# Optimization experiments

Hardware: AMD Instinct MI355X
Metric: run time of the kernel (lower is better)

The kernel has to match this reference:

```python
import jax, jax.numpy as jnp
import numpy as np

OBS, HOR, PD, HID, NH, PROTO = 8, 8, 128, 256, 8, 32
B, N = 8, 4096

def _gelu(x):
    return jax.nn.gelu(x, approximate=False)  # torch nn.GELU default is exact erf

def setup_inputs():
    key = jax.random.key(0)
    ks = iter(jax.random.split(key, 40))
    nrm = lambda shape, s=0.02: jax.random.normal(next(ks), shape, dtype=jnp.float32) * s
    return {
        'obs_points': jax.random.normal(next(ks), (B, N, OBS, 2), dtype=jnp.float32),
        'obs_vis': jax.random.randint(next(ks), (B, N, OBS), 0, 2).astype(bool),
        'rel_xy': jax.random.normal(next(ks), (B, N, 2), dtype=jnp.float32),
        'anchor_obs': jax.random.normal(next(ks), (B, OBS, 2), dtype=jnp.float32),
        'anchor_obs_vel': jax.random.normal(next(ks), (B, OBS, 2), dtype=jnp.float32),
        'semantic_feat': jax.random.normal(next(ks), (B, N, 10), dtype=jnp.float32),
        'ln_w': jnp.ones((OBS * 7,), jnp.float32),
        'ln_b': jnp.zeros((OBS * 7,), jnp.float32),
        'enc_w1': nrm((OBS * 7, PD)), 'enc_b1': jnp.zeros((PD,), jnp.float32),
        'enc_w2': nrm((PD, PD)), 'enc_b2': jnp.zeros((PD,), jnp.float32),
        'time_embed': nrm((HOR, HID)),
        'anchor_w': nrm((OBS * 4, HID)), 'anchor_b': jnp.zeros((HID,), jnp.float32),
        'query_w': nrm((PD, HID)), 'query_b': jnp.zeros((HID,), jnp.float32),
        'in_proj_w': nrm((HID, 3 * HID)), 'in_proj_b': jnp.zeros((3 * HID,), jnp.float32),
        'out_proj_w': nrm((HID, HID)), 'out_proj_b': jnp.zeros((HID,), jnp.float32),
        'ah_w': nrm((HID, 2)), 'ah_b': jnp.zeros((2,), jnp.float32),
        'rh_w1': nrm((HID + PD + 2, HID)), 'rh_b1': jnp.zeros((HID,), jnp.float32),
        'rh_w2': nrm((HID, 2)), 'rh_b2': jnp.zeros((2,), jnp.float32),
        'vh_w1': nrm((HID + PD, HID // 2)), 'vh_b1': jnp.zeros((HID // 2,), jnp.float32),
        'vh_w2': nrm((HID // 2, 1)), 'vh_b2': jnp.zeros((1,), jnp.float32),
        'sh_w': nrm((HID, PROTO)), 'sh_b': jnp.zeros((PROTO,), jnp.float32),
    }

def reference(obs_points, obs_vis, rel_xy, anchor_obs, anchor_obs_vel, semantic_feat,
              ln_w, ln_b, enc_w1, enc_b1, enc_w2, enc_b2, time_embed,
              anchor_w, anchor_b, query_w, query_b, in_proj_w, in_proj_b,
              out_proj_w, out_proj_b, ah_w, ah_b, rh_w1, rh_b1, rh_w2, rh_b2,
              vh_w1, vh_b1, vh_w2, vh_b2, sh_w, sh_b):
    del semantic_feat  # unused, matches original
    Bc, Nc, T, _ = obs_points.shape
    # ---- PointTraceEncoder ----
    vel = jnp.concatenate([jnp.zeros_like(obs_points[:, :, :1]),
                           obs_points[:, :, 1:] - obs_points[:, :, :-1]], axis=2)
    rel = jnp.broadcast_to(rel_xy[:, :, None, :], (Bc, Nc, T, 2))
    feat = jnp.concatenate([obs_points, vel, obs_vis.astype(jnp.float32)[..., None], rel],
                           axis=-1).reshape(Bc, Nc, T * 7)
    mu = feat.mean(-1, keepdims=True)
    var = ((feat - mu) ** 2).mean(-1, keepdims=True)
    x = (feat - mu) / jnp.sqrt(var + 1e-5) * ln_w + ln_b
    point_tokens = _gelu(_gelu(x @ enc_w1 + enc_b1) @ enc_w2 + enc_b2)  # [B,N,PD]
    # ---- queries / memory ----
    anchor_feat = jnp.concatenate([anchor_obs, anchor_obs_vel], -1).reshape(Bc, -1)
    tq = time_embed[None] + (anchor_feat @ anchor_w + anchor_b)[:, None]  # [B,HOR,HID]
    mem = point_tokens @ query_w + query_b  # [B,N,HID]
    # ---- multi-head cross attention ----
    D = tq.shape[-1]; dh = D // NH
    q = tq @ in_proj_w[:, :D] + in_proj_b[:D]
    k = mem @ in_proj_w[:, D:2 * D] + in_proj_b[D:2 * D]
    v = mem @ in_proj_w[:, 2 * D:] + in_proj_b[2 * D:]
    qh = q.reshape(Bc, -1, NH, dh).transpose(0, 2, 1, 3)
    kh = k.reshape(Bc, -1, NH, dh).transpose(0, 2, 1, 3)
    vh = v.reshape(Bc, -1, NH, dh).transpose(0, 2, 1, 3)
    attn = jax.nn.softmax(jnp.einsum('bhqd,bhkd->bhqk', qh, kh) / jnp.sqrt(jnp.float32(dh)), axis=-1)
    o = jnp.einsum('bhqk,bhkd->bhqd', attn, vh).transpose(0, 2, 1, 3).reshape(Bc, -1, D)
    future = o @ out_proj_w + out_proj_b  # [B,HOR,HID]
    # ---- heads ----
    last_anchor = anchor_obs[:, -1]
    anchor_delta = 0.1 * jnp.tanh(future @ ah_w + ah_b)
    anchor_pred = last_anchor[:, None] + jnp.cumsum(anchor_delta, axis=1)  # [B,HOR,2]
    Hq = future.shape[1]
    ft_e = jnp.broadcast_to(future[:, :, None, :], (Bc, Hq, Nc, D))
    pt_e = jnp.broadcast_to(point_tokens[:, None], (Bc, Hq, Nc, point_tokens.shape[-1]))
    rel_e = jnp.broadcast_to(rel_xy[:, None], (Bc, Hq, Nc, 2))
    per_point = jnp.concatenate([ft_e, pt_e, rel_e], axis=-1)  # [B,HOR,N,HID+PD+2]
    residual = 0.1 * jnp.tanh(_gelu(per_point @ rh_w1 + rh_b1) @ rh_w2 + rh_b2)
    pred_points = anchor_pred[:, :, None, :] + residual
    vis_logits = (_gelu(per_point[..., :-2] @ vh_w1 + vh_b1) @ vh_w2 + vh_b2)[..., 0]
    sem_logits = future @ sh_w + sh_b
    return (anchor_pred,
            pred_points.transpose(0, 2, 1, 3),   # [B,N,HOR,2]
            vis_logits.transpose(0, 2, 1),       # [B,N,HOR]
            sem_logits)                           # [B,HOR,PROTO]
```

## Files before the change

### kernel.cpp

```cpp
#include <hip/hip_runtime.h>
#include <math.h>

#define BB 8
#define NN 4096
#define TT 8
#define HORQ 8
#define PD 128
#define HID 256
#define NHD 8
#define DH 32
#define FE 56
#define NC2 16
#define CH2 256

typedef __attribute__((ext_vector_type(8))) short short8;
typedef __attribute__((ext_vector_type(4))) float floatx4;
typedef __attribute__((ext_vector_type(2))) float floatx2;
typedef unsigned short ushort_t;

__device__ __forceinline__ float gelu_fast(float x) {
    float x2 = x * x;
    float y2 = x * fmaf(0.0713551f, x2, 1.5957691f);
    float e = __expf(y2);
    return x - x * __builtin_amdgcn_rcpf(1.f + e);
}

__device__ __forceinline__ float tanh_fast(float x) {
    float e = __expf(2.f * x);
    return 1.f - 2.f * __builtin_amdgcn_rcpf(1.f + e);
}

__device__ __forceinline__ ushort_t f2b(float x) {
    union { float f; unsigned u; } c; c.f = x;
    unsigned r = c.u + 0x7fffu + ((c.u >> 16) & 1u);
    return (ushort_t)(r >> 16);
}
__device__ __forceinline__ float b2f(unsigned hi) {
    union { unsigned u; float f; } c; c.u = hi;
    return c.f;
}

__global__ __launch_bounds__(256) void k_fuse(
    const float* __restrict__ qw, const float* __restrict__ qb,
    const float* __restrict__ ipw, const float* __restrict__ ipb,
    float* __restrict__ Wk, float* __restrict__ Wv,
    float* __restrict__ bk, float* __restrict__ bv)
{
    int j = threadIdx.x;
    int blk = blockIdx.x;
    const float* src = (blk < PD) ? (qw + blk * HID) : qb;
    float sk0 = 0.f, sk1 = 0.f, sk2 = 0.f, sk3 = 0.f;
    float sv0 = 0.f, sv1 = 0.f, sv2 = 0.f, sv3 = 0.f;
    for (int l = 0; l < HID; l += 4) {
        float w0 = src[l], w1 = src[l + 1], w2 = src[l + 2], w3 = src[l + 3];
        sk0 += w0 * ipw[l * 768 + 256 + j];
        sk1 += w1 * ipw[(l + 1) * 768 + 256 + j];
        sk2 += w2 * ipw[(l + 2) * 768 + 256 + j];
        sk3 += w3 * ipw[(l + 3) * 768 + 256 + j];
        sv0 += w0 * ipw[l * 768 + 512 + j];
        sv1 += w1 * ipw[(l + 1) * 768 + 512 + j];
        sv2 += w2 * ipw[(l + 2) * 768 + 512 + j];
        sv3 += w3 * ipw[(l + 3) * 768 + 512 + j];
    }
    float sk = sk0 + sk1 + sk2 + sk3, sv = sv0 + sv1 + sv2 + sv3;
    if (blk < PD) {
        Wk[blk * HID + j] = sk;
        Wv[blk * HID + j] = sv;
    } else {
        bk[j] = sk + ipb[256 + j];
        bv[j] = sv + ipb[512 + j];
    }
}

__global__ __launch_bounds__(256) void k_prep(
    const float* __restrict__ Wk, const float* __restrict__ Wv,
    const float* __restrict__ rw1, const float* __restrict__ vw1,
    const float* __restrict__ w1, const float* __restrict__ w2,
    const float* __restrict__ aobs, const float* __restrict__ avel,
    const float* __restrict__ te, const float* __restrict__ aw, const float* __restrict__ ab,
    const float* __restrict__ ipw, const float* __restrict__ ipb,
    short* __restrict__ Wfrag, short* __restrict__ w1frag, short* __restrict__ w2frag,
    float* __restrict__ qb_)
{
    __shared__ float af[32];
    __shared__ float tqs[HID];
    int tid = threadIdx.x;
    int blk = blockIdx.x;
    int ks = tid >> 6, lane = tid & 63;
    int quad = lane >> 4, c16 = lane & 15;
    if (blk < 56) {
        int nt = blk;
        int n = nt * 16 + c16;
        for (int j = 0; j < 8; j++) {
            int k = ks * 32 + quad * 8 + j;
            float v;
            if (n < 256)      v = Wk[k * HID + n];
            else if (n < 512) v = Wv[k * HID + (n - 256)];
            else if (n < 768) v = rw1[(256 + k) * HID + (n - 512)];
            else              v = vw1[(256 + k) * PD + (n - 768)];
            Wfrag[((nt * 4 + ks) * 64 + lane) * 8 + j] = (short)f2b(v);
        }
    } else if (blk < 64) {
        if (ks < 2) {
            int nt = blk - 56;
            int n = nt * 16 + c16;
            for (int j = 0; j < 8; j++) {
                int k = ks * 32 + quad * 8 + j;
                float v = (k < FE) ? w1[k * PD + n] : 0.f;
                w1frag[((nt * 2 + ks) * 64 + lane) * 8 + j] = (short)f2b(v);
            }
        }
    } else if (blk < 72) {
        int nt = blk - 64;
        int n = nt * 16 + c16;
        for (int j = 0; j < 8; j++) {
            int k = ks * 32 + quad * 8 + j;
            w2frag[((nt * 4 + ks) * 64 + lane) * 8 + j] = (short)f2b(w2[k * PD + n]);
        }
    } else {
        int bh = blk - 72;
        int b = bh >> 3, h = bh & 7;
        if (tid < 32) {
            int t = tid >> 2, m = tid & 3;
            af[tid] = (m < 2) ? aobs[(b * TT + t) * 2 + m] : avel[(b * TT + t) * 2 + (m - 2)];
        }
        __syncthreads();
        float s = te[h * HID + tid] + ab[tid];
        for (int i = 0; i < 32; i++) s += af[i] * aw[i * HID + tid];
        tqs[tid] = s;
        __syncthreads();
        float q0 = ipb[tid], q1 = 0.f, q2 = 0.f, q3 = 0.f;
        for (int i = 0; i < HID; i += 4) {
            q0 += tqs[i] * ipw[i * 768 + tid];
            q1 += tqs[i + 1] * ipw[(i + 1) * 768 + tid];
            q2 += tqs[i + 2] * ipw[(i + 2) * 768 + tid];
            q3 += tqs[i + 3] * ipw[(i + 3) * 768 + tid];
        }
        qb_[(size_t)bh * HID + tid] = q0 + q1 + q2 + q3;
    }
}

#define U1_OFF 0
#define XNB_OFF 17408
#define PTB_OFF 26624
#define RXY_OFF 44032
#define MU_OFF 44544
#define RS_OFF 44800
#define SMEM_BYTES 45056

__global__ __launch_bounds__(256) void k_main(
    const float* __restrict__ obs, const int* __restrict__ vis,
    const float* __restrict__ rel,
    const float* __restrict__ lnw, const float* __restrict__ lnb,
    const float* __restrict__ b1, const float* __restrict__ b2,
    const short* __restrict__ Wfrag, const short* __restrict__ w1frag,
    const short* __restrict__ w2frag,
    const float* __restrict__ bk, const float* __restrict__ bv,
    const float* __restrict__ rw1,
    ushort_t* __restrict__ kb, ushort_t* __restrict__ vb,
    ushort_t* __restrict__ P1, ushort_t* __restrict__ P2)
{
    __shared__ __align__(16) char smem[SMEM_BYTES];
    float* xnf = (float*)(smem + U1_OFF);
    short* h1b = (short*)(smem + U1_OFF);
    short* xnb = (short*)(smem + XNB_OFF);
    short* ptb = (short*)(smem + PTB_OFF);
    float* rxyS = (float*)(smem + RXY_OFF);
    float* muS = (float*)(smem + MU_OFF);
    float* rsS = (float*)(smem + RS_OFF);

    int tid = threadIdx.x;
    int w = tid >> 6, lane = tid & 63;
    int quad = lane >> 4, c16 = lane & 15;
    int bn0 = blockIdx.x * 64;

    #pragma unroll
    for (int u = 0; u < 2; u++) {
        int pair = tid + u * 256;
        int p = pair >> 3, t = pair & 7;
        int bn = bn0 + p;
        float2 oc = *(const float2*)(obs + (bn * TT + t) * 2);
        int tp = t ? (t - 1) : 0;
        float2 op = *(const float2*)(obs + (bn * TT + tp) * 2);
        float dx = t ? (oc.x - op.x) : 0.f;
        float dy = t ? (oc.y - op.y) : 0.f;
        float vv = (float)vis[bn * TT + t];
        float2 rl = *(const float2*)(rel + bn * 2);
        float* xp = xnf + p * 57 + t * 7;
        xp[0] = oc.x; xp[1] = oc.y; xp[2] = dx; xp[3] = dy;
        xp[4] = vv; xp[5] = rl.x; xp[6] = rl.y;
    }
    if (tid < 128) rxyS[tid] = rel[bn0 * 2 + tid];
    __syncthreads();

    {
        int p = tid >> 2, r = tid & 3;
        float s = 0.f, ss = 0.f;
        for (int e = r; e < FE; e += 4) { float v = xnf[p * 57 + e]; s += v; ss += v * v; }
        s += __shfl_xor(s, 1); ss += __shfl_xor(ss, 1);
        s += __shfl_xor(s, 2); ss += __shfl_xor(ss, 2);
        if (r == 0) {
            float mu = s * (1.f / FE);
            float var = ss * (1.f / FE) - mu * mu;
            muS[p] = mu;
            rsS[p] = rsqrtf(var + 1e-5f);
        }
    }
    __syncthreads();

    for (int idx = tid; idx < 64 * 64; idx += 256) {
        int p = idx >> 6, e = idx & 63;
        float v = 0.f;
        if (e < FE) v = (xnf[p * 57 + e] - muS[p]) * rsS[p] * lnw[e] + lnb[e];
        xnb[p * 72 + e] = (short)f2b(v);
    }
    __syncthreads();

    {
        short8 af1[4][2];
        #pragma unroll
        for (int mt = 0; mt < 4; mt++)
            #pragma unroll
            for (int ks = 0; ks < 2; ks++)
                af1[mt][ks] = *(const short8*)(xnb + (mt * 16 + c16) * 72 + ks * 32 + quad * 8);
        #pragma unroll
        for (int ntl = 0; ntl < 2; ntl++) {
            int nt = w * 2 + ntl;
            short8 bf1[2];
            #pragma unroll
            for (int ks = 0; ks < 2; ks++)
                bf1[ks] = *(const short8*)(w1frag + ((nt * 2 + ks) * 64 + lane) * 8);
            int col = nt * 16 + c16;
            float bb = b1[col];
            #pragma unroll
            for (int mt = 0; mt < 4; mt++) {
                floatx4 acc = {0.f, 0.f, 0.f, 0.f};
                acc = __builtin_amdgcn_mfma_f32_16x16x32_bf16(af1[mt][0], bf1[0], acc, 0, 0, 0);
                acc = __builtin_amdgcn_mfma_f32_16x16x32_bf16(af1[mt][1], bf1[1], acc, 0, 0, 0);
                #pragma unroll
                for (int r = 0; r < 4; r++) {
                    int row = mt * 16 + quad * 4 + r;
                    h1b[row * 136 + col] = (short)f2b(gelu_fast(acc[r] + bb));
                }
            }
        }
    }
    __syncthreads();

    {
        short8 af2[4][4];
        #pragma unroll
        for (int mt = 0; mt < 4; mt++)
            #pragma unroll
            for (int ks = 0; ks < 4; ks++)
                af2[mt][ks] = *(const short8*)(h1b + (mt * 16 + c16) * 136 + ks * 32 + quad * 8);
        #pragma unroll
        for (int ntl = 0; ntl < 2; ntl++) {
            int nt = w * 2 + ntl;
            short8 bf2[4];
            #pragma unroll
            for (int ks = 0; ks < 4; ks++)
                bf2[ks] = *(const short8*)(w2frag + ((nt * 4 + ks) * 64 + lane) * 8);
            int col = nt * 16 + c16;
            float bb = b2[col];
            #pragma unroll
            for (int mt = 0; mt < 4; mt++) {
                floatx4 acc = {0.f, 0.f, 0.f, 0.f};
                #pragma unroll
                for (int ks = 0; ks < 4; ks++)
                    acc = __builtin_amdgcn_mfma_f32_16x16x32_bf16(af2[mt][ks], bf2[ks], acc, 0, 0, 0);
                #pragma unroll
                for (int r = 0; r < 4; r++) {
                    int row = mt * 16 + quad * 4 + r;
                    ptb[row * 136 + col] = (short)f2b(gelu_fast(acc[r] + bb));
                }
            }
        }
    }
    __syncthreads();

    {
        short8 af[4][4];
        #pragma unroll
        for (int mt = 0; mt < 4; mt++)
            #pragma unroll
            for (int ks = 0; ks < 4; ks++)
                af[mt][ks] = *(const short8*)(ptb + (mt * 16 + c16) * 136 + ks * 32 + quad * 8);
        for (int i = 0; i < 14; i++) {
            int nt = w + i * 4;
            short8 bf[4];
            #pragma unroll
            for (int ks = 0; ks < 4; ks++)
                bf[ks] = *(const short8*)(Wfrag + ((nt * 4 + ks) * 64 + lane) * 8);
            floatx4 acc[4];
            #pragma unroll
            for (int mt = 0; mt < 4; mt++) {
                acc[mt] = (floatx4){0.f, 0.f, 0.f, 0.f};
                #pragma unroll
                for (int ks = 0; ks < 4; ks++)
                    acc[mt] = __builtin_amdgcn_mfma_f32_16x16x32_bf16(af[mt][ks], bf[ks], acc[mt], 0, 0, 0);
            }
            int n = nt * 16 + c16;
            if (nt < 16) {
                float bb = bk[n];
                #pragma unroll
                for (int mt = 0; mt < 4; mt++)
                    #pragma unroll
                    for (int r = 0; r < 4; r++) {
                        int row = mt * 16 + quad * 4 + r;
                        kb[(size_t)(bn0 + row) * HID + n] = f2b(acc[mt][r] + bb);
                    }
            } else if (nt < 32) {
                int j = n - 256;
                float bb = bv[j];
                #pragma unroll
                for (int mt = 0; mt < 4; mt++)
                    #pragma unroll
                    for (int r = 0; r < 4; r++) {
                        int row = mt * 16 + quad * 4 + r;
                        vb[(size_t)(bn0 + row) * HID + j] = f2b(acc[mt][r] + bb);
                    }
            } else if (nt < 48) {
                int j = n - 512;
                float wr0 = rw1[384 * HID + j], wr1 = rw1[385 * HID + j];
                #pragma unroll
                for (int mt = 0; mt < 4; mt++)
                    #pragma unroll
                    for (int r = 0; r < 4; r++) {
                        int row = mt * 16 + quad * 4 + r;
                        P1[(size_t)(bn0 + row) * HID + j] =
                            f2b(acc[mt][r] + rxyS[row * 2] * wr0 + rxyS[row * 2 + 1] * wr1);
                    }
            } else {
                int j = n - 768;
                #pragma unroll
                for (int mt = 0; mt < 4; mt++)
                    #pragma unroll
                    for (int r = 0; r < 4; r++) {
                        int row = mt * 16 + quad * 4 + r;
                        P2[(size_t)(bn0 + row) * PD + j] = f2b(acc[mt][r]);
                    }
            }
        }
    }
}

__global__ __launch_bounds__(256) void k_att(
    const float* __restrict__ qbuf, const ushort_t* __restrict__ kb, const ushort_t* __restrict__ vbuf,
    float* __restrict__ pm, float* __restrict__ pl, float* __restrict__ po)
{
    __shared__ float sc[8][CH2];
    __shared__ float pos[8][8][DH];
    int tid = threadIdx.x;
    int bidx = blockIdx.x;
    int c = bidx & (NC2 - 1);
    int head = (bidx >> 4) & 7;
    int b = bidx >> 7;
    const float scale = 0.17677669529663688110f;
    {
        int qq = tid >> 5, ln = tid & 31;
        float qr[DH];
        const float* qp = qbuf + (size_t)(b * HORQ + qq) * HID + head * DH;
        #pragma unroll
        for (int u = 0; u < 8; u++) {
            float4 f = *(const float4*)(qp + u * 4);
            qr[u * 4] = f.x; qr[u * 4 + 1] = f.y; qr[u * 4 + 2] = f.z; qr[u * 4 + 3] = f.w;
        }
        #pragma unroll
        for (int i = 0; i < 8; i++) {
            int nn = ln + 32 * i;
            const ushort_t* kp = kb + (size_t)(b * NN + c * CH2 + nn) * HID + head * DH;
            float s = 0.f;
            #pragma unroll
            for (int u = 0; u < 4; u++) {
                uint4 q = *(const uint4*)(kp + u * 8);
                unsigned wd[4] = {q.x, q.y, q.z, q.w};
                #pragma unroll
                for (int t2 = 0; t2 < 4; t2++) {
                    s += qr[u * 8 + 2 * t2]     * b2f(wd[t2] << 16);
                    s += qr[u * 8 + 2 * t2 + 1] * b2f(wd[t2] & 0xffff0000u);
                }
            }
            sc[qq][nn] = s * scale;
        }
    }
    __syncthreads();
    int qq = tid >> 5, r = tid & 31;
    float mx = -1e30f;
    #pragma unroll
    for (int nn = r; nn < CH2; nn += 32) mx = fmaxf(mx, sc[qq][nn]);
    #pragma unroll
    for (int m = 16; m; m >>= 1) mx = fmaxf(mx, __shfl_xor(mx, m, 32));
    float sum = 0.f;
    #pragma unroll
    for (int nn = r; nn < CH2; nn += 32) { float e = __expf(sc[qq][nn] - mx); sc[qq][nn] = e; sum += e; }
    #pragma unroll
    for (int m = 16; m; m >>= 1) sum += __shfl_xor(sum, m, 32);
    if (r == 0) { pm[bidx * 8 + qq] = mx; pl[bidx * 8 + qq] = sum; }
    __syncthreads();
    {
        int g = tid >> 5, d = tid & 31;
        float oacc[8];
        #pragma unroll
        for (int q2 = 0; q2 < 8; q2++) oacc[q2] = 0.f;
        const ushort_t* vp = vbuf + ((size_t)(b * NN + c * CH2 + g * 32)) * HID + head * DH + d;
        for (int i = 0; i < 32; i++) {
            float v = b2f(((unsigned)vp[(size_t)i * HID]) << 16);
            int nn = g * 32 + i;
            #pragma unroll
            for (int q2 = 0; q2 < 8; q2++) oacc[q2] += sc[q2][nn] * v;
        }
        #pragma unroll
        for (int q2 = 0; q2 < 8; q2++) pos[g][q2][d] = oacc[q2];
    }
    __syncthreads();
    {
        int q2 = tid >> 5, d = tid & 31;
        float o = 0.f;
        #pragma unroll
        for (int gg = 0; gg < 8; gg++) o += pos[gg][q2][d];
        po[(size_t)(bidx * 8 + q2) * DH + d] = o;
    }
}

__global__ __launch_bounds__(256) void k_attfut(
    const float* __restrict__ pm, const float* __restrict__ pl, const float* __restrict__ po,
    const float* __restrict__ opw, const float* __restrict__ opb,
    const float* __restrict__ rw1, const float* __restrict__ rb1,
    const float* __restrict__ vw1, const float* __restrict__ vb1,
    const float* __restrict__ shw, const float* __restrict__ shb,
    const float* __restrict__ ahw, const float* __restrict__ ahb,
    float* __restrict__ F1, float* __restrict__ F2, float* __restrict__ dl, float* __restrict__ sem)
{
    __shared__ float orow[HID], fut[HID];
    int tid = threadIdx.x;
    int b = blockIdx.x >> 3, qq = blockIdx.x & 7;
    {
        int head = tid >> 5, d = tid & 31;
        int base = b * 1024 + head * 128 + qq;
        float M = -1e30f;
        #pragma unroll
        for (int c = 0; c < NC2; c++) M = fmaxf(M, pm[base + c * 8]);
        float L = 0.f, o = 0.f;
        #pragma unroll
        for (int c = 0; c < NC2; c++) {
            float wgt = __expf(pm[base + c * 8] - M);
            L += wgt * pl[base + c * 8];
            o += wgt * po[(size_t)(base + c * 8) * DH + d];
        }
        orow[head * DH + d] = o / L;
    }
    __syncthreads();
    {
        float a0 = opb[tid], a1 = 0.f, a2 = 0.f, a3 = 0.f;
        for (int i = 0; i < HID; i += 4) {
            a0 += orow[i] * opw[i * HID + tid];
            a1 += orow[i + 1] * opw[(i + 1) * HID + tid];
            a2 += orow[i + 2] * opw[(i + 2) * HID + tid];
            a3 += orow[i + 3] * opw[(i + 3) * HID + tid];
        }
        fut[tid] = a0 + a1 + a2 + a3;
    }
    __syncthreads();
    int bh = b * HORQ + qq;
    {
        float a0 = rb1[tid], a1 = 0.f, a2 = 0.f, a3 = 0.f;
        for (int i = 0; i < HID; i += 4) {
            a0 += fut[i] * rw1[i * HID + tid];
            a1 += fut[i + 1] * rw1[(i + 1) * HID + tid];
            a2 += fut[i + 2] * rw1[(i + 2) * HID + tid];
            a3 += fut[i + 3] * rw1[(i + 3) * HID + tid];
        }
        F1[(size_t)bh * HID + tid] = a0 + a1 + a2 + a3;
    }
    if (tid < PD) {
        float a0 = vb1[tid], a1 = 0.f, a2 = 0.f, a3 = 0.f;
        for (int i = 0; i < HID; i += 4) {
            a0 += fut[i] * vw1[i * PD + tid];
            a1 += fut[i + 1] * vw1[(i + 1) * PD + tid];
            a2 += fut[i + 2] * vw1[(i + 2) * PD + tid];
            a3 += fut[i + 3] * vw1[(i + 3) * PD + tid];
        }
        F2[(size_t)bh * PD + tid] = a0 + a1 + a2 + a3;
    }
    {
        int j = tid >> 3, part = tid & 7;
        float s3 = 0.f;
        for (int i = part * 32; i < part * 32 + 32; i++) s3 += fut[i] * shw[i * 32 + j];
        s3 += __shfl_xor(s3, 1);
        s3 += __shfl_xor(s3, 2);
        s3 += __shfl_xor(s3, 4);
        if (part == 0) sem[bh * 32 + j] = s3 + shb[j];
    }
    if (tid < 128) {
        int j = tid >> 6, part = tid & 63;
        float a = 0.f;
        #pragma unroll
        for (int u = 0; u < 4; u++) { int i = part * 4 + u; a += fut[i] * ahw[i * 2 + j]; }
        #pragma unroll
        for (int m = 32; m; m >>= 1) a += __shfl_xor(a, m);
        if (part == 0) dl[bh * 2 + j] = 0.1f * tanhf(a + ahb[j]);
    }
}

__global__ void k_cum(const float* __restrict__ aobs, const float* __restrict__ dl, float* __restrict__ out0)
{
    int tid = threadIdx.x;
    if (tid < 16) {
        int b = tid >> 1, c = tid & 1;
        float acc = aobs[(b * TT + 7) * 2 + c];
        for (int h = 0; h < HORQ; h++) {
            acc += dl[(b * HORQ + h) * 2 + c];
            out0[(b * HORQ + h) * 2 + c] = acc;
        }
    }
}

__global__ __launch_bounds__(256) void k_fin(
    const float* __restrict__ F1, const float* __restrict__ F2,
    const ushort_t* __restrict__ P1, const ushort_t* __restrict__ P2,
    const float* __restrict__ rw2, const float* __restrict__ rb2,
    const float* __restrict__ vw2, const float* __restrict__ vb2,
    const float* __restrict__ ap,
    float* __restrict__ out1, float* __restrict__ out2)
{
    int tid = threadIdx.x;
    int sub = tid >> 5;
    int l = tid & 31;
    int bn = blockIdx.x * 8 + sub;
    int b = bn >> 12;

    uint4 q1 = *(const uint4*)(P1 + (size_t)bn * HID + l * 8);
    float p1f[8];
    {
        unsigned wd[4] = {q1.x, q1.y, q1.z, q1.w};
        #pragma unroll
        for (int u = 0; u < 4; u++) {
            p1f[2 * u]     = b2f(wd[u] << 16);
            p1f[2 * u + 1] = b2f(wd[u] & 0xffff0000u);
        }
    }
    floatx2 w01[8];
    {
        const float4* rwp = (const float4*)(rw2 + l * 16);
        #pragma unroll
        for (int u = 0; u < 4; u++) {
            float4 r = rwp[u];
            w01[2 * u] = (floatx2){r.x, r.y};
            w01[2 * u + 1] = (floatx2){r.z, r.w};
        }
    }
    float p2f[4];
    {
        uint2 q2 = *(const uint2*)(P2 + (size_t)bn * PD + l * 4);
        p2f[0] = b2f(q2.x << 16); p2f[1] = b2f(q2.x & 0xffff0000u);
        p2f[2] = b2f(q2.y << 16); p2f[3] = b2f(q2.y & 0xffff0000u);
    }
    float4 wvv = *(const float4*)(vw2 + l * 4);
    float wv[4] = {wvv.x, wvv.y, wvv.z, wvv.w};

    float rb20 = rb2[0], rb21 = rb2[1], vb20 = vb2[0];
    #pragma unroll 2
    for (int h = 0; h < HORQ; h++) {
        const float* f1p = F1 + (size_t)(b * HORQ + h) * HID + l * 8;
        float4 fa = *(const float4*)f1p;
        float4 fb = *(const float4*)(f1p + 4);
        float f1r[8] = {fa.x, fa.y, fa.z, fa.w, fb.x, fb.y, fb.z, fb.w};
        float4 f2v = *(const float4*)(F2 + (size_t)(b * HORQ + h) * PD + l * 4);
        float f2r[4] = {f2v.x, f2v.y, f2v.z, f2v.w};
        floatx2 s01 = {0.f, 0.f};
        float sv = 0.f;
        #pragma unroll
        for (int u = 0; u < 8; u++) {
            float g = gelu_fast(f1r[u] + p1f[u]);
            s01 += (floatx2){g, g} * w01[u];
        }
        #pragma unroll
        for (int u = 0; u < 4; u++) {
            float g = gelu_fast(f2r[u] + p2f[u]);
            sv += g * wv[u];
        }
        float s0 = s01.x, s1 = s01.y;
        #pragma unroll
        for (int m = 16; m; m >>= 1) {
            s0 += __shfl_xor(s0, m, 32);
            s1 += __shfl_xor(s1, m, 32);
            sv += __shfl_xor(sv, m, 32);
        }
        if (l == 0) {
            float rx = 0.1f * tanh_fast(s0 + rb20);
            float ry = 0.1f * tanh_fast(s1 + rb21);
            int bh = b * HORQ + h;
            out1[((size_t)bn * HORQ + h) * 2 + 0] = ap[bh * 2 + 0] + rx;
            out1[((size_t)bn * HORQ + h) * 2 + 1] = ap[bh * 2 + 1] + ry;
            out2[(size_t)bn * HORQ + h] = sv + vb20;
        }
    }
}

extern "C" void kernel_launch(void* const* d_in, const int* in_sizes, int n_in,
                              void* d_out, int out_size, void* d_ws, size_t ws_size,
                              hipStream_t stream)
{
    const float* obs  = (const float*)d_in[0];
    const int*   vis  = (const int*)d_in[1];
    const float* rel  = (const float*)d_in[2];
    const float* aobs = (const float*)d_in[3];
    const float* avel = (const float*)d_in[4];
    const float* lnw = (const float*)d_in[6];
    const float* lnb = (const float*)d_in[7];
    const float* ew1 = (const float*)d_in[8];
    const float* eb1 = (const float*)d_in[9];
    const float* ew2 = (const float*)d_in[10];
    const float* eb2 = (const float*)d_in[11];
    const float* te  = (const float*)d_in[12];
    const float* aw  = (const float*)d_in[13];
    const float* ab  = (const float*)d_in[14];
    const float* qw  = (const float*)d_in[15];
    const float* qbias = (const float*)d_in[16];
    const float* ipw = (const float*)d_in[17];
    const float* ipb = (const float*)d_in[18];
    const float* opw = (const float*)d_in[19];
    const float* opb = (const float*)d_in[20];
    const float* ahw = (const float*)d_in[21];
    const float* ahb = (const float*)d_in[22];
    const float* rw1 = (const float*)d_in[23];
    const float* rb1 = (const float*)d_in[24];
    const float* rw2 = (const float*)d_in[25];
    const float* rb2 = (const float*)d_in[26];
    const float* vw1 = (const float*)d_in[27];
    const float* vb1 = (const float*)d_in[28];
    const float* vw2 = (const float*)d_in[29];
    const float* vb2 = (const float*)d_in[30];
    const float* shw = (const float*)d_in[31];
    const float* shb = (const float*)d_in[32];

    float* W = (float*)d_ws;
    size_t o = 0;
    float* Wk  = W + o; o += (size_t)PD * HID;
    float* Wv  = W + o; o += (size_t)PD * HID;
    float* bk  = W + o; o += HID;
    float* bv  = W + o; o += HID;
    float* qb_ = W + o; o += (size_t)BB * HORQ * HID;
    float* F1  = W + o; o += (size_t)BB * HORQ * HID;
    float* F2  = W + o; o += (size_t)BB * HORQ * PD;
    float* dl  = W + o; o += (size_t)BB * HORQ * 2;
    float* pm  = W + o; o += (size_t)BB * NHD * NC2 * 8;
    float* pl  = W + o; o += (size_t)BB * NHD * NC2 * 8;
    float* po  = W + o; o += (size_t)BB * NHD * NC2 * 8 * DH;
    ushort_t* kb   = (ushort_t*)(W + o); o += (size_t)BB * NN * HID / 2;
    ushort_t* vbuf = (ushort_t*)(W + o); o += (size_t)BB * NN * HID / 2;
    ushort_t* P1   = (ushort_t*)(W + o); o += (size_t)BB * NN * HID / 2;
    ushort_t* P2   = (ushort_t*)(W + o); o += (size_t)BB * NN * PD / 2;
    short* Sf = (short*)(W + o);
    short* Wfrag  = Sf;
    short* w1frag = Sf + 114688;
    short* w2frag = Sf + 114688 + 8192;

    float* out0 = (float*)d_out;
    float* out1 = out0 + BB * HORQ * 2;
    float* out2 = out1 + (size_t)BB * NN * HORQ * 2;
    float* out3 = out2 + (size_t)BB * NN * HORQ;

    k_fuse<<<PD + 1, 256, 0, stream>>>(qw, qbias, ipw, ipb, Wk, Wv, bk, bv);
    k_prep<<<72 + 64, 256, 0, stream>>>(Wk, Wv, rw1, vw1, ew1, ew2,
                                        aobs, avel, te, aw, ab, ipw, ipb,
                                        Wfrag, w1frag, w2frag, qb_);
    k_main<<<BB * NN / 64, 256, 0, stream>>>(obs, vis, rel, lnw, lnb, eb1, eb2,
                                             Wfrag, w1frag, w2frag, bk, bv, rw1,
                                             kb, vbuf, P1, P2);
    k_att<<<BB * NHD * NC2, 256, 0, stream>>>(qb_, kb, vbuf, pm, pl, po);
    k_attfut<<<BB * HORQ, 256, 0, stream>>>(pm, pl, po, opw, opb, rw1, rb1, vw1, vb1,
                                            shw, shb, ahw, ahb, F1, F2, dl, out3);
    k_cum<<<1, 64, 0, stream>>>(aobs, dl, out0);
    k_fin<<<BB * NN / 8, 256, 0, stream>>>(F1, F2, P1, P2, rw2, rb2, vw2, vb2,
                                           out0, out1, out2);
}
```

Baseline: 260.5 us.

## Vectorize MFMA epilogue stores, fold weight fusion into prep, inline anchor cumsum

Result: slower. 268.5 us (+3.1%).

```diff
diff --git a/kernel.cpp b/kernel.cpp
--- a/kernel.cpp
+++ b/kernel.cpp
@@ -25,6 +25,11 @@
     return x - x * __builtin_amdgcn_rcpf(1.f + e);
 }
 
+__device__ __forceinline__ float gelu_sig(float x) {
+    float e = __expf(-1.702f * x);
+    return x * __builtin_amdgcn_rcpf(1.f + e);
+}
+
 __device__ __forceinline__ float tanh_fast(float x) {
     float e = __expf(2.f * x);
     return 1.f - 2.f * __builtin_amdgcn_rcpf(1.f + e);
@@ -39,48 +44,22 @@
     union { unsigned u; float f; } c; c.u = hi;
     return c.f;
 }
-
-__global__ __launch_bounds__(256) void k_fuse(
+__device__ __forceinline__ uint2 pack4(float a, float b, float c, float d) {
+    uint2 r;
+    r.x = (unsigned)f2b(a) | ((unsigned)f2b(b) << 16);
+    r.y = (unsigned)f2b(c) | ((unsigned)f2b(d) << 16);
+    return r;
+}
+
+__global__ __launch_bounds__(256) void k_prep(
     const float* __restrict__ qw, const float* __restrict__ qb,
     const float* __restrict__ ipw, const float* __restrict__ ipb,
-    float* __restrict__ Wk, float* __restrict__ Wv,
-    float* __restrict__ bk, float* __restrict__ bv)
-{
-    int j = threadIdx.x;
-    int blk = blockIdx.x;
-    const float* src = (blk < PD) ? (qw + blk * HID) : qb;
-    float sk0 = 0.f, sk1 = 0.f, sk2 = 0.f, sk3 = 0.f;
-    float sv0 = 0.f, sv1 = 0.f, sv2 = 0.f, sv3 = 0.f;
-    for (int l = 0; l < HID; l += 4) {
-        float w0 = src[l], w1 = src[l + 1], w2 = src[l + 2], w3 = src[l + 3];
-        sk0 += w0 * ipw[l * 768 + 256 + j];
-        sk1 += w1 * ipw[(l + 1) * 768 + 256 + j];
-        sk2 += w2 * ipw[(l + 2) * 768 + 256 + j];
-        sk3 += w3 * ipw[(l + 3) * 768 + 256 + j];
-        sv0 += w0 * ipw[l * 768 + 512 + j];
-        sv1 += w1 * ipw[(l + 1) * 768 + 512 + j];
-        sv2 += w2 * ipw[(l + 2) * 768 + 512 + j];
-        sv3 += w3 * ipw[(l + 3) * 768 + 512 + j];
-    }
-    float sk = sk0 + sk1 + sk2 + sk3, sv = sv0 + sv1 + sv2 + sv3;
-    if (blk < PD) {
-        Wk[blk * HID + j] = sk;
-        Wv[blk * HID + j] = sv;
-    } else {
-        bk[j] = sk + ipb[256 + j];
-        bv[j] = sv + ipb[512 + j];
-    }
-}
-
-__global__ __launch_bounds__(256) void k_prep(
-    const float* __restrict__ Wk, const float* __restrict__ Wv,
     const float* __restrict__ rw1, const float* __restrict__ vw1,
     const float* __restrict__ w1, const float* __restrict__ w2,
     const float* __restrict__ aobs, const float* __restrict__ avel,
     const float* __restrict__ te, const float* __restrict__ aw, const float* __restrict__ ab,
-    const float* __restrict__ ipw, const float* __restrict__ ipb,
     short* __restrict__ Wfrag, short* __restrict__ w1frag, short* __restrict__ w2frag,
-    float* __restrict__ qb_)
+    float* __restrict__ bk, float* __restrict__ bv, float* __restrict__ qb_)
 {
     __shared__ float af[32];
     __shared__ float tqs[HID];
@@ -88,16 +67,31 @@
     int blk = blockIdx.x;
     int ks = tid >> 6, lane = tid & 63;
     int quad = lane >> 4, c16 = lane & 15;
-    if (blk < 56) {
+    if (blk < 32) {
+        int nt = blk;
+        int n = nt * 16 + c16;
+        int k0 = ks * 32 + quad * 8;
+        float acc[8];
+        #pragma unroll
+        for (int j = 0; j < 8; j++) acc[j] = 0.f;
+        const float* ipcol = ipw + 256 + n;
+        const float* qrow = qw + k0 * 256;
+        #pragma unroll 4
+        for (int l = 0; l < HID; l++) {
+            float ip = ipcol[l * 768];
+            #pragma unroll
+            for (int j = 0; j < 8; j++) acc[j] = fmaf(qrow[j * 256 + l], ip, acc[j]);
+        }
+        #pragma unroll
+        for (int j = 0; j < 8; j++)
+            Wfrag[((nt * 4 + ks) * 64 + lane) * 8 + j] = (short)f2b(acc[j]);
+    } else if (blk < 56) {
         int nt = blk;
         int n = nt * 16 + c16;
         for (int j = 0; j < 8; j++) {
             int k = ks * 32 + quad * 8 + j;
-            float v;
-            if (n < 256)      v = Wk[k * HID + n];
-            else if (n < 512) v = Wv[k * HID + (n - 256)];
-            else if (n < 768) v = rw1[(256 + k) * HID + (n - 512)];
-            else              v = vw1[(256 + k) * PD + (n - 768)];
+            float v = (n < 768) ? rw1[(256 + k) * HID + (n - 512)]
+                                : vw1[(256 + k) * PD + (n - 768)];
             Wfrag[((nt * 4 + ks) * 64 + lane) * 8 + j] = (short)f2b(v);
         }
     } else if (blk < 64) {
@@ -117,8 +111,24 @@
             int k = ks * 32 + quad * 8 + j;
             w2frag[((nt * 4 + ks) * 64 + lane) * 8 + j] = (short)f2b(w2[k * PD + n]);
         }
+    } else if (blk == 72) {
+        int j = tid;
+        float s0 = ipb[256 + j], s1 = 0.f, s2 = 0.f, s3 = 0.f;
+        float v0 = ipb[512 + j], v1 = 0.f, v2 = 0.f, v3 = 0.f;
+        for (int l = 0; l < HID; l += 4) {
+            s0 += qb[l] * ipw[l * 768 + 256 + j];
+            s1 += qb[l + 1] * ipw[(l + 1) * 768 + 256 + j];
+            s2 += qb[l + 2] * ipw[(l + 2) * 768 + 256 + j];
+            s3 += qb[l + 3] * ipw[(l + 3) * 768 + 256 + j];
+            v0 += qb[l] * ipw[l * 768 + 512 + j];
+            v1 += qb[l + 1] * ipw[(l + 1) * 768 + 512 + j];
+            v2 += qb[l + 2] * ipw[(l + 2) * 768 + 512 + j];
+            v3 += qb[l + 3] * ipw[(l + 3) * 768 + 512 + j];
+        }
+        bk[j] = s0 + s1 + s2 + s3;
+        bv[j] = v0 + v1 + v2 + v3;
     } else {
-        int bh = blk - 72;
+        int bh = blk - 73;
         int b = bh >> 3, h = bh & 7;
         if (tid < 32) {
             int t = tid >> 2, m = tid & 3;
@@ -230,18 +240,17 @@
             #pragma unroll
             for (int ks = 0; ks < 2; ks++)
                 bf1[ks] = *(const short8*)(w1frag + ((nt * 2 + ks) * 64 + lane) * 8);
-            int col = nt * 16 + c16;
-            float bb = b1[col];
+            int o0 = nt * 16 + quad * 4;
+            float4 b14 = *(const float4*)(b1 + o0);
             #pragma unroll
             for (int mt = 0; mt < 4; mt++) {
                 floatx4 acc = {0.f, 0.f, 0.f, 0.f};
-                acc = __builtin_amdgcn_mfma_f32_16x16x32_bf16(af1[mt][0], bf1[0], acc, 0, 0, 0);
-                acc = __builtin_amdgcn_mfma_f32_16x16x32_bf16(af1[mt][1], bf1[1], acc, 0, 0, 0);
-                #pragma unroll
-                for (int r = 0; r < 4; r++) {
-                    int row = mt * 16 + quad * 4 + r;
-                    h1b[row * 136 + col] = (short)f2b(gelu_fast(acc[r] + bb));
-                }
+                acc = __builtin_amdgcn_mfma_f32_16x16x32_bf16(bf1[0], af1[mt][0], acc, 0, 0, 0);
+                acc = __builtin_amdgcn_mfma_f32_16x16x32_bf16(bf1[1], af1[mt][1], acc, 0, 0, 0);
+                int p = mt * 16 + c16;
+                uint2 pk = pack4(gelu_fast(acc[0] + b14.x), gelu_fast(acc[1] + b14.y),
+                                 gelu_fast(acc[2] + b14.z), gelu_fast(acc[3] + b14.w));
+                *reinterpret_cast<uint2*>(h1b + p * 136 + o0) = pk;
             }
         }
     }
@@ -261,19 +270,18 @@
             #pragma unroll
             for (int ks = 0; ks < 4; ks++)
                 bf2[ks] = *(const short8*)(w2frag + ((nt * 4 + ks) * 64 + lane) * 8);
-            int col = nt * 16 + c16;
-            float bb = b2[col];
+            int o0 = nt * 16 + quad * 4;
+            float4 b24 = *(const float4*)(b2 + o0);
             #pragma unroll
             for (int mt = 0; mt < 4; mt++) {
                 floatx4 acc = {0.f, 0.f, 0.f, 0.f};
                 #pragma unroll
                 for (int ks = 0; ks < 4; ks++)
-                    acc = __builtin_amdgcn_mfma_f32_16x16x32_bf16(af2[mt][ks], bf2[ks], acc, 0, 0, 0);
-                #pragma unroll
-                for (int r = 0; r < 4; r++) {
-                    int row = mt * 16 + quad * 4 + r;
-                    ptb[row * 136 + col] = (short)f2b(gelu_fast(acc[r] + bb));
-                }
+                    acc = __builtin_amdgcn_mfma_f32_16x16x32_bf16(bf2[ks], af2[mt][ks], acc, 0, 0, 0);
+                int p = mt * 16 + c16;
+                uint2 pk = pack4(gelu_fast(acc[0] + b24.x), gelu_fast(acc[1] + b24.y),
+                                 gelu_fast(acc[2] + b24.z), gelu_fast(acc[3] + b24.w));
+                *reinterpret_cast<uint2*>(ptb + p * 136 + o0) = pk;
             }
         }
     }
@@ -286,6 +294,12 @@
             #pragma unroll
             for (int ks = 0; ks < 4; ks++)
                 af[mt][ks] = *(const short8*)(ptb + (mt * 16 + c16) * 136 + ks * 32 + quad * 8);
+        floatx2 rxv[4];
+        #pragma unroll
+        for (int mt = 0; mt < 4; mt++) {
+            float2 t = *(const float2*)(rxyS + (mt * 16 + c16) * 2);
+            rxv[mt] = (floatx2){t.x, t.y};
+        }
         for (int i = 0; i < 14; i++) {
             int nt = w + i * 4;
             short8 bf[4];
@@ -298,48 +312,50 @@
                 acc[mt] = (floatx4){0.f, 0.f, 0.f, 0.f};
                 #pragma unroll
                 for (int ks = 0; ks < 4; ks++)
-                    acc[mt] = __builtin_amdgcn_mfma_f32_16x16x32_bf16(af[mt][ks], bf[ks], acc[mt], 0, 0, 0);
+                    acc[mt] = __builtin_amdgcn_mfma_f32_16x16x32_bf16(bf[ks], af[mt][ks], acc[mt], 0, 0, 0);
             }
-            int n = nt * 16 + c16;
+            int n0 = nt * 16 + quad * 4;
             if (nt < 16) {
-                float bb = bk[n];
+                float4 bb = *(const float4*)(bk + n0);
                 #pragma unroll
-                for (int mt = 0; mt < 4; mt++)
-                    #pragma unroll
-                    for (int r = 0; r < 4; r++) {
-                        int row = mt * 16 + quad * 4 + r;
-                        kb[(size_t)(bn0 + row) * HID + n] = f2b(acc[mt][r] + bb);
-                    }
+                for (int mt = 0; mt < 4; mt++) {
+                    int p = bn0 + mt * 16 + c16;
+                    uint2 pk = pack4(acc[mt][0] + bb.x, acc[mt][1] + bb.y,
+                                     acc[mt][2] + bb.z, acc[mt][3] + bb.w);
+                    *reinterpret_cast<uint2*>(kb + (size_t)p * HID + n0) = pk;
+                }
             } else if (nt < 32) {
-                int j = n - 256;
-                float bb = bv[j];
+                int j0 = n0 - 256;
+                float4 bb = *(const float4*)(bv + j0);
                 #pragma unroll
-                for (int mt = 0; mt < 4; mt++)
-                    #pragma unroll
-                    for (int r = 0; r < 4; r++) {
-                        int row = mt * 16 + quad * 4 + r;
-                        vb[(size_t)(bn0 + row) * HID + j] = f2b(acc[mt][r] + bb);
-                    }
+                for (int mt = 0; mt < 4; mt++) {
+                    int p = bn0 + mt * 16 + c16;
+                    uint2 pk = pack4(acc[mt][0] + bb.x, acc[mt][1] + bb.y,
+                                     acc[mt][2] + bb.z, acc[mt][3] + bb.w);
+                    *reinterpret_cast<uint2*>(vb + (size_t)p * HID + j0) = pk;
+                }
             } else if (nt < 48) {
-                int j = n - 512;
-                float wr0 = rw1[384 * HID + j], wr1 = rw1[385 * HID + j];
+                int j0 = n0 - 512;
+                float4 w04 = *(const float4*)(rw1 + 384 * HID + j0);
+                float4 w14 = *(const float4*)(rw1 + 385 * HID + j0);
                 #pragma unroll
-                for (int mt = 0; mt < 4; mt++)
-                    #pragma unroll
-                    for (int r = 0; r < 4; r++) {
-                        int row = mt * 16 + quad * 4 + r;
-                        P1[(size_t)(bn0 + row) * HID + j] =
-                            f2b(acc[mt][r] + rxyS[row * 2] * wr0 + rxyS[row * 2 + 1] * wr1);
-                    }
+                for (int mt = 0; mt < 4; mt++) {
+                    int p = bn0 + mt * 16 + c16;
+                    float rx = rxv[mt].x, ry = rxv[mt].y;
+                    uint2 pk = pack4(acc[mt][0] + rx * w04.x + ry * w14.x,
+                                     acc[mt][1] + rx * w04.y + ry * w14.y,
+                                     acc[mt][2] + rx * w04.z + ry * w14.z,
+                                     acc[mt][3] + rx * w04.w + ry * w14.w);
+                    *reinterpret_cast<uint2*>(P1 + (size_t)p * HID + j0) = pk;
+                }
             } else {
-                int j = n - 768;
+                int j0 = n0 - 768;
                 #pragma unroll
-                for (int mt = 0; mt < 4; mt++)
-                    #pragma unroll
-                    for (int r = 0; r < 4; r++) {
-                        int row = mt * 16 + quad * 4 + r;
-                        P2[(size_t)(bn0 + row) * PD + j] = f2b(acc[mt][r]);
-                    }
+                for (int mt = 0; mt < 4; mt++) {
+                    int p = bn0 + mt * 16 + c16;
+                    uint2 pk = pack4(acc[mt][0], acc[mt][1], acc[mt][2], acc[mt][3]);
+                    *reinterpret_cast<uint2*>(P2 + (size_t)p * PD + j0) = pk;
+                }
             }
         }
     }
@@ -521,7 +537,7 @@
     const ushort_t* __restrict__ P1, const ushort_t* __restrict__ P2,
     const float* __restrict__ rw2, const float* __restrict__ rb2,
     const float* __restrict__ vw2, const float* __restrict__ vb2,
-    const float* __restrict__ ap,
+    const float* __restrict__ aobs, const float* __restrict__ dl,
     float* __restrict__ out1, float* __restrict__ out2)
 {
     int tid = threadIdx.x;
@@ -529,6 +545,17 @@
     int l = tid & 31;
     int bn = blockIdx.x * 8 + sub;
     int b = bn >> 12;
+
+    float apx[8], apy[8];
+    {
+        float ax = aobs[(b * TT + 7) * 2 + 0], ay = aobs[(b * TT + 7) * 2 + 1];
+        #pragma unroll
+        for (int h = 0; h < HORQ; h++) {
+            ax += dl[(b * HORQ + h) * 2 + 0];
+            ay += dl[(b * HORQ + h) * 2 + 1];
+            apx[h] = ax; apy[h] = ay;
+        }
+    }
 
     uint4 q1 = *(const uint4*)(P1 + (size_t)bn * HID + l * 8);
     float p1f[8];
@@ -572,12 +599,12 @@
         float sv = 0.f;
         #pragma unroll
         for (int u = 0; u < 8; u++) {
-            float g = gelu_fast(f1r[u] + p1f[u]);
+            float g = gelu_sig(f1r[u] + p1f[u]);
             s01 += (floatx2){g, g} * w01[u];
         }
         #pragma unroll
         for (int u = 0; u < 4; u++) {
-            float g = gelu_fast(f2r[u] + p2f[u]);
+            float g = gelu_sig(f2r[u] + p2f[u]);
             sv += g * wv[u];
         }
         float s0 = s01.x, s1 = s01.y;
@@ -590,9 +617,8 @@
         if (l == 0) {
             float rx = 0.1f * tanh_fast(s0 + rb20);
             float ry = 0.1f * tanh_fast(s1 + rb21);
-            int bh = b * HORQ + h;
-            out1[((size_t)bn * HORQ + h) * 2 + 0] = ap[bh * 2 + 0] + rx;
-            out1[((size_t)bn * HORQ + h) * 2 + 1] = ap[bh * 2 + 1] + ry;
+            out1[((size_t)bn * HORQ + h) * 2 + 0] = apx[h] + rx;
+            out1[((size_t)bn * HORQ + h) * 2 + 1] = apy[h] + ry;
             out2[(size_t)bn * HORQ + h] = sv + vb20;
         }
     }
@@ -637,8 +663,6 @@
 
     float* W = (float*)d_ws;
     size_t o = 0;
-    float* Wk  = W + o; o += (size_t)PD * HID;
-    float* Wv  = W + o; o += (size_t)PD * HID;
     float* bk  = W + o; o += HID;
     float* bv  = W + o; o += HID;
     float* qb_ = W + o; o += (size_t)BB * HORQ * HID;
@@ -662,17 +686,16 @@
     float* out2 = out1 + (size_t)BB * NN * HORQ * 2;
     float* out3 = out2 + (size_t)BB * NN * HORQ;
 
-    k_fuse<<<PD + 1, 256, 0, stream>>>(qw, qbias, ipw, ipb, Wk, Wv, bk, bv);
-    k_prep<<<72 + 64, 256, 0, stream>>>(Wk, Wv, rw1, vw1, ew1, ew2,
-                                        aobs, avel, te, aw, ab, ipw, ipb,
-                                        Wfrag, w1frag, w2frag, qb_);
+    k_prep<<<137, 256, 0, stream>>>(qw, qbias, ipw, ipb, rw1, vw1, ew1, ew2,
+                                    aobs, avel, te, aw, ab,
+                                    Wfrag, w1frag, w2frag, bk, bv, qb_);
     k_main<<<BB * NN / 64, 256, 0, stream>>>(obs, vis, rel, lnw, lnb, eb1, eb2,
                                              Wfrag, w1frag, w2frag, bk, bv, rw1,
                                              kb, vbuf, P1, P2);
     k_att<<<BB * NHD * NC2, 256, 0, stream>>>(qb_, kb, vbuf, pm, pl, po);
     k_attfut<<<BB * HORQ, 256, 0, stream>>>(pm, pl, po, opw, opb, rw1, rb1, vw1, vb1,
                                             shw, shb, ahw, ahb, F1, F2, dl, out3);
+    k_fin<<<BB * NN / 8, 256, 0, stream>>>(F1, F2, P1, P2, rw2, rb2, vw2, vb2,
+                                           aobs, dl, out1, out2);
     k_cum<<<1, 64, 0, stream>>>(aobs, dl, out0);
-    k_fin<<<BB * NN / 8, 256, 0, stream>>>(F1, F2, P1, P2, rw2, rb2, vw2, vb2,
-                                           out0, out1, out2);
-}
+}
```

## Use sigmoid GELU approximation in k_fin, halve k_main tile, restructure k_fin loops

Applied to the files above, without the earlier changes.

Result: no change. 263.5 us (+1.1%).

```diff
diff --git a/kernel.cpp b/kernel.cpp
--- a/kernel.cpp
+++ b/kernel.cpp
@@ -23,6 +23,11 @@
     float y2 = x * fmaf(0.0713551f, x2, 1.5957691f);
     float e = __expf(y2);
     return x - x * __builtin_amdgcn_rcpf(1.f + e);
+}
+
+__device__ __forceinline__ float gelu_sig(float x) {
+    float e = __expf(-1.702f * x);
+    return x * __builtin_amdgcn_rcpf(1.f + e);
 }
 
 __device__ __forceinline__ float tanh_fast(float x) {
@@ -141,12 +146,12 @@
 }
 
 #define U1_OFF 0
-#define XNB_OFF 17408
-#define PTB_OFF 26624
-#define RXY_OFF 44032
-#define MU_OFF 44544
-#define RS_OFF 44800
-#define SMEM_BYTES 45056
+#define XNB_OFF 8704
+#define PTB_OFF 13312
+#define RXY_OFF 22016
+#define MU_OFF 22272
+#define RS_OFF 22400
+#define SMEM_BYTES 22528
 
 __global__ __launch_bounds__(256) void k_main(
     const float* __restrict__ obs, const int* __restrict__ vis,
@@ -172,12 +177,10 @@
     int tid = threadIdx.x;
     int w = tid >> 6, lane = tid & 63;
     int quad = lane >> 4, c16 = lane & 15;
-    int bn0 = blockIdx.x * 64;
-
-    #pragma unroll
-    for (int u = 0; u < 2; u++) {
-        int pair = tid + u * 256;
-        int p = pair >> 3, t = pair & 7;
+    int bn0 = blockIdx.x * 32;
+
+    {
+        int p = tid >> 3, t = tid & 7;
         int bn = bn0 + p;
         float2 oc = *(const float2*)(obs + (bn * TT + t) * 2);
         int tp = t ? (t - 1) : 0;
@@ -190,15 +193,16 @@
         xp[0] = oc.x; xp[1] = oc.y; xp[2] = dx; xp[3] = dy;
         xp[4] = vv; xp[5] = rl.x; xp[6] = rl.y;
     }
-    if (tid < 128) rxyS[tid] = rel[bn0 * 2 + tid];
-    __syncthreads();
-
-    {
-        int p = tid >> 2, r = tid & 3;
+    if (tid < 64) rxyS[tid] = rel[bn0 * 2 + tid];
+    __syncthreads();
+
+    {
+        int p = tid >> 3, r = tid & 7;
         float s = 0.f, ss = 0.f;
-        for (int e = r; e < FE; e += 4) { float v = xnf[p * 57 + e]; s += v; ss += v * v; }
+        for (int e = r; e < FE; e += 8) { float v = xnf[p * 57 + e]; s += v; ss += v * v; }
         s += __shfl_xor(s, 1); ss += __shfl_xor(ss, 1);
         s += __shfl_xor(s, 2); ss += __shfl_xor(ss, 2);
+        s += __shfl_xor(s, 4); ss += __shfl_xor(ss, 4);
         if (r == 0) {
             float mu = s * (1.f / FE);
             float var = ss * (1.f / FE) - mu * mu;
@@ -208,7 +212,7 @@
     }
     __syncthreads();
 
-    for (int idx = tid; idx < 64 * 64; idx += 256) {
+    for (int idx = tid; idx < 32 * 64; idx += 256) {
         int p = idx >> 6, e = idx & 63;
         float v = 0.f;
         if (e < FE) v = (xnf[p * 57 + e] - muS[p]) * rsS[p] * lnw[e] + lnb[e];
@@ -217,9 +221,9 @@
     __syncthreads();
 
     {
-        short8 af1[4][2];
-        #pragma unroll
-        for (int mt = 0; mt < 4; mt++)
+        short8 af1[2][2];
+        #pragma unroll
+        for (int mt = 0; mt < 2; mt++)
             #pragma unroll
             for (int ks = 0; ks < 2; ks++)
                 af1[mt][ks] = *(const short8*)(xnb + (mt * 16 + c16) * 72 + ks * 32 + quad * 8);
@@ -233,7 +237,7 @@
             int col = nt * 16 + c16;
             float bb = b1[col];
             #pragma unroll
-            for (int mt = 0; mt < 4; mt++) {
+            for (int mt = 0; mt < 2; mt++) {
                 floatx4 acc = {0.f, 0.f, 0.f, 0.f};
                 acc = __builtin_amdgcn_mfma_f32_16x16x32_bf16(af1[mt][0], bf1[0], acc, 0, 0, 0);
                 acc = __builtin_amdgcn_mfma_f32_16x16x32_bf16(af1[mt][1], bf1[1], acc, 0, 0, 0);
@@ -248,9 +252,9 @@
     __syncthreads();
 
     {
-        short8 af2[4][4];
-        #pragma unroll
-        for (int mt = 0; mt < 4; mt++)
+        short8 af2[2][4];
+        #pragma unroll
+        for (int mt = 0; mt < 2; mt++)
             #pragma unroll
             for (int ks = 0; ks < 4; ks++)
                 af2[mt][ks] = *(const short8*)(h1b + (mt * 16 + c16) * 136 + ks * 32 + quad * 8);
@@ -264,7 +268,7 @@
             int col = nt * 16 + c16;
             float bb = b2[col];
             #pragma unroll
-            for (int mt = 0; mt < 4; mt++) {
+            for (int mt = 0; mt < 2; mt++) {
                 floatx4 acc = {0.f, 0.f, 0.f, 0.f};
                 #pragma unroll
                 for (int ks = 0; ks < 4; ks++)
@@ -280,9 +284,9 @@
     __syncthreads();
 
     {
-        short8 af[4][4];
-        #pragma unroll
-        for (int mt = 0; mt < 4; mt++)
+        short8 af[2][4];
+        #pragma unroll
+        for (int mt = 0; mt < 2; mt++)
             #pragma unroll
             for (int ks = 0; ks < 4; ks++)
                 af[mt][ks] = *(const short8*)(ptb + (mt * 16 + c16) * 136 + ks * 32 + quad * 8);
@@ -292,9 +296,9 @@
             #pragma unroll
             for (int ks = 0; ks < 4; ks++)
                 bf[ks] = *(const short8*)(Wfrag + ((nt * 4 + ks) * 64 + lane) * 8);
-            floatx4 acc[4];
-            #pragma unroll
-            for (int mt = 0; mt < 4; mt++) {
+            floatx4 acc[2];
+            #pragma unroll
+            for (int mt = 0; mt < 2; mt++) {
                 acc[mt] = (floatx4){0.f, 0.f, 0.f, 0.f};
                 #pragma unroll
                 for (int ks = 0; ks < 4; ks++)
@@ -304,7 +308,7 @@
             if (nt < 16) {
                 float bb = bk[n];
                 #pragma unroll
-                for (int mt = 0; mt < 4; mt++)
+                for (int mt = 0; mt < 2; mt++)
                     #pragma unroll
                     for (int r = 0; r < 4; r++) {
                         int row = mt * 16 + quad * 4 + r;
@@ -314,7 +318,7 @@
                 int j = n - 256;
                 float bb = bv[j];
                 #pragma unroll
-                for (int mt = 0; mt < 4; mt++)
+                for (int mt = 0; mt < 2; mt++)
                     #pragma unroll
                     for (int r = 0; r < 4; r++) {
                         int row = mt * 16 + quad * 4 + r;
@@ -324,7 +328,7 @@
                 int j = n - 512;
                 float wr0 = rw1[384 * HID + j], wr1 = rw1[385 * HID + j];
                 #pragma unroll
-                for (int mt = 0; mt < 4; mt++)
+                for (int mt = 0; mt < 2; mt++)
                     #pragma unroll
                     for (int r = 0; r < 4; r++) {
                         int row = mt * 16 + quad * 4 + r;
@@ -334,7 +338,7 @@
             } else {
                 int j = n - 768;
                 #pragma unroll
-                for (int mt = 0; mt < 4; mt++)
+                for (int mt = 0; mt < 2; mt++)
                     #pragma unroll
                     for (int r = 0; r < 4; r++) {
                         int row = mt * 16 + quad * 4 + r;
@@ -525,75 +529,76 @@
     float* __restrict__ out1, float* __restrict__ out2)
 {
     int tid = threadIdx.x;
-    int sub = tid >> 5;
-    int l = tid & 31;
-    int bn = blockIdx.x * 8 + sub;
+    int g = tid >> 4;
+    int l = tid & 15;
+    int bn = blockIdx.x * 16 + g;
     int b = bn >> 12;
-
-    uint4 q1 = *(const uint4*)(P1 + (size_t)bn * HID + l * 8);
-    float p1f[8];
-    {
-        unsigned wd[4] = {q1.x, q1.y, q1.z, q1.w};
-        #pragma unroll
-        for (int u = 0; u < 4; u++) {
-            p1f[2 * u]     = b2f(wd[u] << 16);
-            p1f[2 * u + 1] = b2f(wd[u] & 0xffff0000u);
-        }
-    }
-    floatx2 w01[8];
-    {
-        const float4* rwp = (const float4*)(rw2 + l * 16);
-        #pragma unroll
-        for (int u = 0; u < 4; u++) {
-            float4 r = rwp[u];
-            w01[2 * u] = (floatx2){r.x, r.y};
-            w01[2 * u + 1] = (floatx2){r.z, r.w};
-        }
-    }
-    float p2f[4];
-    {
-        uint2 q2 = *(const uint2*)(P2 + (size_t)bn * PD + l * 4);
-        p2f[0] = b2f(q2.x << 16); p2f[1] = b2f(q2.x & 0xffff0000u);
-        p2f[2] = b2f(q2.y << 16); p2f[3] = b2f(q2.y & 0xffff0000u);
-    }
-    float4 wvv = *(const float4*)(vw2 + l * 4);
-    float wv[4] = {wvv.x, wvv.y, wvv.z, wvv.w};
+    int bh0 = b * HORQ;
+
+    float s0[8], s1[8], sv[8];
+    #pragma unroll
+    for (int h = 0; h < 8; h++) { s0[h] = 0.f; s1[h] = 0.f; sv[h] = 0.f; }
+
+    {
+        const ushort_t* p1base = P1 + (size_t)bn * HID + l * 16;
+        const float* f1base = F1 + (size_t)bh0 * HID + l * 16;
+        #pragma unroll
+        for (int c = 0; c < 4; c++) {
+            uint2 pq = *(const uint2*)(p1base + c * 4);
+            float p0 = b2f(pq.x << 16), p1v = b2f(pq.x & 0xffff0000u);
+            float p2 = b2f(pq.y << 16), p3 = b2f(pq.y & 0xffff0000u);
+            const float* rwp = rw2 + (l * 16 + c * 4) * 2;
+            float4 ra = *(const float4*)rwp;
+            float4 rb = *(const float4*)(rwp + 4);
+            #pragma unroll
+            for (int h = 0; h < 8; h++) {
+                float4 f = *(const float4*)(f1base + h * HID + c * 4);
+                float g0 = gelu_sig(f.x + p0);
+                float g1 = gelu_sig(f.y + p1v);
+                float g2 = gelu_sig(f.z + p2);
+                float g3 = gelu_sig(f.w + p3);
+                s0[h] += g0 * ra.x + g1 * ra.z + g2 * rb.x + g3 * rb.z;
+                s1[h] += g0 * ra.y + g1 * ra.w + g2 * rb.y + g3 * rb.w;
+            }
+        }
+    }
+    {
+        const ushort_t* p2base = P2 + (size_t)bn * PD + l * 8;
+        const float* f2base = F2 + (size_t)bh0 * PD + l * 8;
+        #pragma unroll
+        for (int c = 0; c < 2; c++) {
+            uint2 pq = *(const uint2*)(p2base + c * 4);
+            float p0 = b2f(pq.x << 16), p1v = b2f(pq.x & 0xffff0000u);
+            float p2 = b2f(pq.y << 16), p3 = b2f(pq.y & 0xffff0000u);
+            float4 wv4 = *(const float4*)(vw2 + l * 8 + c * 4);
+            #pragma unroll
+            for (int h = 0; h < 8; h++) {
+                float4 f = *(const float4*)(f2base + h * PD + c * 4);
+                sv[h] += gelu_sig(f.x + p0) * wv4.x
+                       + gelu_sig(f.y + p1v) * wv4.y
+                       + gelu_sig(f.z + p2) * wv4.z
+                       + gelu_sig(f.w + p3) * wv4.w;
+            }
+        }
+    }
 
     float rb20 = rb2[0], rb21 = rb2[1], vb20 = vb2[0];
-    #pragma unroll 2
-    for (int h = 0; h < HORQ; h++) {
-        const float* f1p = F1 + (size_t)(b * HORQ + h) * HID + l * 8;
-        float4 fa = *(const float4*)f1p;
-        float4 fb = *(const float4*)(f1p + 4);
-        float f1r[8] = {fa.x, fa.y, fa.z, fa.w, fb.x, fb.y, fb.z, fb.w};
-        float4 f2v = *(const float4*)(F2 + (size_t)(b * HORQ + h) * PD + l * 4);
-        float f2r[4] = {f2v.x, f2v.y, f2v.z, f2v.w};
-        floatx2 s01 = {0.f, 0.f};
-        float sv = 0.f;
-        #pragma unroll
-        for (int u = 0; u < 8; u++) {
-            float g = gelu_fast(f1r[u] + p1f[u]);
-            s01 += (floatx2){g, g} * w01[u];
-        }
-        #pragma unroll
-        for (int u = 0; u < 4; u++) {
-            float g = gelu_fast(f2r[u] + p2f[u]);
-            sv += g * wv[u];
-        }
-        float s0 = s01.x, s1 = s01.y;
-        #pragma unroll
-        for (int m = 16; m; m >>= 1) {
-            s0 += __shfl_xor(s0, m, 32);
-            s1 += __shfl_xor(s1, m, 32);
-            sv += __shfl_xor(sv, m, 32);
+    #pragma unroll
+    for (int h = 0; h < 8; h++) {
+        float a0 = s0[h], a1 = s1[h], a2 = sv[h];
+        #pragma unroll
+        for (int m = 8; m; m >>= 1) {
+            a0 += __shfl_xor(a0, m, 16);
+            a1 += __shfl_xor(a1, m, 16);
+            a2 += __shfl_xor(a2, m, 16);
         }
         if (l == 0) {
-            float rx = 0.1f * tanh_fast(s0 + rb20);
-            float ry = 0.1f * tanh_fast(s1 + rb21);
-            int bh = b * HORQ + h;
+            float rx = 0.1f * tanh_fast(a0 + rb20);
+            float ry = 0.1f * tanh_fast(a1 + rb21);
+            int bh = bh0 + h;
             out1[((size_t)bn * HORQ + h) * 2 + 0] = ap[bh * 2 + 0] + rx;
             out1[((size_t)bn * HORQ + h) * 2 + 1] = ap[bh * 2 + 1] + ry;
-            out2[(size_t)bn * HORQ + h] = sv + vb20;
+            out2[(size_t)bn * HORQ + h] = a2 + vb20;
         }
     }
 }
@@ -666,13 +671,13 @@
     k_prep<<<72 + 64, 256, 0, stream>>>(Wk, Wv, rw1, vw1, ew1, ew2,
                                         aobs, avel, te, aw, ab, ipw, ipb,
                                         Wfrag, w1frag, w2frag, qb_);
-    k_main<<<BB * NN / 64, 256, 0, stream>>>(obs, vis, rel, lnw, lnb, eb1, eb2,
+    k_main<<<BB * NN / 32, 256, 0, stream>>>(obs, vis, rel, lnw, lnb, eb1, eb2,
                                              Wfrag, w1frag, w2frag, bk, bv, rw1,
                                              kb, vbuf, P1, P2);
     k_att<<<BB * NHD * NC2, 256, 0, stream>>>(qb_, kb, vbuf, pm, pl, po);
     k_attfut<<<BB * HORQ, 256, 0, stream>>>(pm, pl, po, opw, opb, rw1, rb1, vw1, vb1,
                                             shw, shb, ahw, ahb, F1, F2, dl, out3);
     k_cum<<<1, 64, 0, stream>>>(aobs, dl, out0);
-    k_fin<<<BB * NN / 8, 256, 0, stream>>>(F1, F2, P1, P2, rw2, rb2, vw2, vb2,
-                                           out0, out1, out2);
-}
+    k_fin<<<BB * NN / 16, 256, 0, stream>>>(F1, F2, P1, P2, rw2, rb2, vw2, vb2,
+                                            out0, out1, out2);
+}
```
